# Performance work log

Hardware: AMD Instinct MI355X
Metric: run time of the kernel (lower is better)

## Reference

```python
import jax, jax.numpy as jnp
import numpy as np
import math

NUM_HEADS = 16
HEAD_DIM = 64  # 1024 / 16

def setup_inputs() -> dict:
    key = jax.random.key(0)
    k1, k2, k3 = jax.random.split(key, 3)
    B, S, D = 2, 2048, 1024
    scale = 1.0 / math.sqrt(D)
    return {
        "hidden_states": jax.random.normal(k1, (B, S, D), dtype=jnp.float32),
        "attention_mask": jnp.ones((B, S), dtype=jnp.int32),
        "Wq": jax.random.normal(k2, (D, D), dtype=jnp.float32) * scale,
        "bq": jnp.zeros((D,), dtype=jnp.float32),
        "Wk": jax.random.normal(k3, (D, D), dtype=jnp.float32) * scale,
        "bk": jnp.zeros((D,), dtype=jnp.float32),
    }

def _split_heads(x):
    # [B, S, D] -> [B, H, S, dh]
    B, S, D = x.shape
    return x.reshape(B, S, NUM_HEADS, HEAD_DIM).transpose(0, 2, 1, 3)

def reference(hidden_states, attention_mask, Wq, bq, Wk, bk):
    q = _split_heads(hidden_states @ Wq + bq)           # [B,H,S,dh]
    k = _split_heads(hidden_states @ Wk + bk)           # [B,H,S,dh]
    k = jax.nn.log_sigmoid(q) + q + k                   # fused logsigmoid on q
    k = jax.nn.log_sigmoid(k)                           # second logsigmoid
    # scores = q @ (-k^T) / sqrt(dh)
    scores = -jnp.einsum('bhqd,bhkd->bhqk', q, k) / math.sqrt(HEAD_DIM)
    # mask broadcast [B,1,S,1]: masks QUERY rows (faithful to original)
    mask = (attention_mask[:, None, :, None] == 0)
    scores = jnp.where(mask, -10000.0, scores)
    probs = jax.nn.softmax(scores, axis=-1)             # [B,H,S,S]
    # note: value == query_layer in this module
    ctx = jnp.einsum('bhqk,bhkd->bhqd', probs, q)       # [B,H,S,dh]
    B, H, S, dh = ctx.shape
    return ctx.transpose(0, 2, 1, 3).reshape(B, S, H * dh)
```

## Files before the change

kernel.cpp:

```cpp
#include <hip/hip_runtime.h>
#include <hip/hip_bf16.h>
#include <math.h>

#define B_  2
#define S_  2048
#define D_  1024
#define H_  16
#define DH_ 64
#define M_  (B_ * S_)

typedef __attribute__((ext_vector_type(8))) short bf16x8;
typedef __attribute__((ext_vector_type(4))) float f32x4;
typedef __attribute__((ext_vector_type(16))) float f32x16;
typedef __attribute__((ext_vector_type(2))) unsigned u32x2;

__device__ __forceinline__ float fast_exp2(float x) {
  return __builtin_amdgcn_exp2f(x);
}

__device__ __forceinline__ unsigned short f2bf(float f) {
  union { float f; unsigned u; } c; c.f = f;
  unsigned u = c.u;
  return (unsigned short)((u + 0x7FFFu + ((u >> 16) & 1u)) >> 16);
}

__device__ __forceinline__ unsigned cvtpk(float lo, float hi) {
  unsigned r;
  asm("v_cvt_pk_bf16_f32 %0, %1, %2" : "=v"(r) : "v"(lo), "v"(hi));
  return r;
}

__device__ __forceinline__ void plswap(unsigned &x, unsigned &y) {
  u32x2 r = __builtin_amdgcn_permlane32_swap(x, y, false, false);
  x = r[0]; y = r[1];
}

__device__ __forceinline__ float logsig(float x) {
  const float e = __expf(-fabsf(x));
  return fminf(x, 0.f) - __logf(1.f + e);
}

__global__ __launch_bounds__(256) void prep_w(
    const float* __restrict__ Wq, const float* __restrict__ Wk,
    unsigned short* __restrict__ WqT, unsigned short* __restrict__ WkT)
{
  __shared__ unsigned short T[64][72];
  const int tid = threadIdx.x;
  const int k0 = blockIdx.x * 64;
  const int n0 = blockIdx.y * 64;
  const float* W = blockIdx.z ? Wk : Wq;
  unsigned short* WT = blockIdx.z ? WkT : WqT;

  const int kr = tid >> 2, nc = (tid & 3) * 16;
  #pragma unroll
  for (int i = 0; i < 4; i++) {
    const float4 v = *(const float4*)&W[(size_t)(k0 + kr) * D_ + n0 + nc + i * 4];
    T[nc + i * 4 + 0][kr] = f2bf(v.x);
    T[nc + i * 4 + 1][kr] = f2bf(v.y);
    T[nc + i * 4 + 2][kr] = f2bf(v.z);
    T[nc + i * 4 + 3][kr] = f2bf(v.w);
  }
  __syncthreads();
  const int nr = tid >> 2, kc = (tid & 3) * 16;
  const uint4 a = *(const uint4*)&T[nr][kc];
  const uint4 b = *(const uint4*)&T[nr][kc + 8];
  *(uint4*)&WT[(size_t)(n0 + nr) * D_ + k0 + kc] = a;
  *(uint4*)&WT[(size_t)(n0 + nr) * D_ + k0 + kc + 8] = b;
}

__global__ __launch_bounds__(512, 4) void proj_kernel(
    const float* __restrict__ hs,
    const unsigned short* __restrict__ WqT, const unsigned short* __restrict__ WkT,
    const float* __restrict__ bqv, const float* __restrict__ bkv,
    unsigned short* __restrict__ K2b, unsigned short* __restrict__ QT)
{
  __shared__ unsigned short Ash[128][72];
  __shared__ unsigned short Bsh[2][64][72];

  const int tid  = threadIdx.x;
  const int w    = tid >> 6;
  const int lane = tid & 63;
  const int quad = lane >> 4;
  const int l16  = lane & 15;
  const int m0 = blockIdx.x * 128;
  const int n0 = blockIdx.y * 64;

  float bqs[4], bks[4];
  #pragma unroll
  for (int nt = 0; nt < 4; nt++) {
    bqs[nt] = bqv[n0 + nt * 16 + l16];
    bks[nt] = bkv[n0 + nt * 16 + l16];
  }

  f32x4 accQ[4], accK[4];
  #pragma unroll
  for (int nt = 0; nt < 4; nt++) {
    accQ[nt] = (f32x4){0.f, 0.f, 0.f, 0.f};
    accK[nt] = (f32x4){0.f, 0.f, 0.f, 0.f};
  }

  const int am = tid >> 2, ac = (tid & 3) * 16;
  const int bn = tid >> 3, bc = (tid & 7) * 8;

  float4 Af[4];
  uint4 Bq, Bk;
  {
    const size_t ra = (size_t)(m0 + am) * D_ + ac;
    #pragma unroll
    for (int i = 0; i < 4; i++) Af[i] = *(const float4*)&hs[ra + i * 4];
    const size_t rb = (size_t)(n0 + bn) * D_ + bc;
    Bq = *(const uint4*)&WqT[rb];
    Bk = *(const uint4*)&WkT[rb];
  }

  for (int k0 = 0; k0 < D_; k0 += 64) {
    if (k0) __syncthreads();
    {
      uint4 t0, t1;
      t0.x = cvtpk(Af[0].x, Af[0].y);  t0.y = cvtpk(Af[0].z, Af[0].w);
      t0.z = cvtpk(Af[1].x, Af[1].y);  t0.w = cvtpk(Af[1].z, Af[1].w);
      t1.x = cvtpk(Af[2].x, Af[2].y);  t1.y = cvtpk(Af[2].z, Af[2].w);
      t1.z = cvtpk(Af[3].x, Af[3].y);  t1.w = cvtpk(Af[3].z, Af[3].w);
      *(uint4*)&Ash[am][ac]     = t0;
      *(uint4*)&Ash[am][ac + 8] = t1;
    }
    *(uint4*)&Bsh[0][bn][bc] = Bq;
    *(uint4*)&Bsh[1][bn][bc] = Bk;
    __syncthreads();

    if (k0 + 64 < D_) {
      const size_t ra = (size_t)(m0 + am) * D_ + (k0 + 64) + ac;
      #pragma unroll
      for (int i = 0; i < 4; i++) Af[i] = *(const float4*)&hs[ra + i * 4];
      const size_t rb = (size_t)(n0 + bn) * D_ + (k0 + 64) + bc;
      Bq = *(const uint4*)&WqT[rb];
      Bk = *(const uint4*)&WkT[rb];
    }

    #pragma unroll
    for (int kk = 0; kk < 2; kk++) {
      const bf16x8 af = *(const bf16x8*)&Ash[w * 16 + l16][kk * 32 + quad * 8];
      #pragma unroll
      for (int nt = 0; nt < 4; nt++) {
        const bf16x8 bq = *(const bf16x8*)&Bsh[0][nt * 16 + l16][kk * 32 + quad * 8];
        const bf16x8 bk = *(const bf16x8*)&Bsh[1][nt * 16 + l16][kk * 32 + quad * 8];
        accQ[nt] = __builtin_amdgcn_mfma_f32_16x16x32_bf16(af, bq, accQ[nt], 0, 0, 0);
        accK[nt] = __builtin_amdgcn_mfma_f32_16x16x32_bf16(af, bk, accK[nt], 0, 0, 0);
      }
    }
  }
  __syncthreads();

  unsigned short* Qt = &Bsh[0][0][0];
  #pragma unroll
  for (int nt = 0; nt < 4; nt++) {
    float qv[4];
    #pragma unroll
    for (int r = 0; r < 4; r++) {
      const float q  = accQ[nt][r] + bqs[nt];
      const float kr = accK[nt][r] + bks[nt];
      const float k2 = logsig(logsig(q) + q + kr);
      const int m = m0 + w * 16 + quad * 4 + r;
      K2b[(size_t)m * D_ + n0 + nt * 16 + l16] = f2bf(k2);
      qv[r] = q;
    }
    const ushort4 qu = {f2bf(qv[0]), f2bf(qv[1]), f2bf(qv[2]), f2bf(qv[3])};
    *(ushort4*)&Qt[(nt * 16 + l16) * 136 + w * 16 + quad * 4] = qu;
  }
  __syncthreads();
  {
    const int dr = tid >> 3, mc = (tid & 7) * 16;
    #pragma unroll
    for (int i = 0; i < 2; i++) {
      const uint4 v = *(const uint4*)&Qt[dr * 136 + mc + i * 8];
      *(uint4*)&QT[(size_t)(n0 + dr) * M_ + m0 + mc + i * 8] = v;
    }
  }
}

__global__ __launch_bounds__(1024) void attn_kernel(
    const unsigned short* __restrict__ QT,
    const unsigned short* __restrict__ K2b,
    const int* __restrict__ mask,
    float* __restrict__ out)
{
  __shared__ unsigned short Qa [256][72];
  __shared__ unsigned short K2s[64][72];
  __shared__ unsigned short Vt [64][72];

  const int tid  = threadIdx.x;
  const int w    = tid >> 6;
  const int lane = tid & 63;
  const int r31  = lane & 31;
  const int hi   = lane >> 5;
  const int hi8  = hi * 8;
  const int qsub = w & 7;
  const int ksel = w >> 3;

  const int qt = blockIdx.x;
  const int bh = blockIdx.y;
  const int b = bh >> 4, h = bh & 15;
  const size_t qrow0 = (size_t)b * S_ + (size_t)qt * 256;
  const size_t krow0 = (size_t)b * S_;
  const size_t trow  = (size_t)h * 64;

  const int rr = tid >> 4, cc = (tid & 15) * 4;
  uint2 kreg, vreg;
  kreg = *(const uint2*)&K2b[(krow0 + rr) * D_ + trow + cc];
  vreg = *(const uint2*)&QT [(trow + rr) * M_ + krow0 + cc];

  {
    const int dr = tid >> 4, qg = tid & 15;
    const int qc = qg * 16;
    const int dcol = dr ^ ((qg & 7) << 3);
    #pragma unroll
    for (int i = 0; i < 2; i++) {
      const uint4 v = *(const uint4*)&QT[(trow + dr) * M_ + qrow0 + qc + i * 8];
      const unsigned short* p = (const unsigned short*)&v;
      #pragma unroll
      for (int j = 0; j < 8; j++) Qa[qc + i * 8 + j][dcol] = p[j];
    }
  }
  __syncthreads();

  bf16x8 qfrag[4];
  {
    const int qrow = qsub * 32 + r31;
    const int g7 = (qrow >> 4) & 7;
    #pragma unroll
    for (int s = 0; s < 4; s++)
      qfrag[s] = *(const bf16x8*)&Qa[qrow][(s * 16 + hi8) ^ (g7 << 3)];
  }

  const float c2 = (mask[qrow0 + qsub * 32 + r31] != 0) ? -0.18033688f : 0.f;
  float rl = 0.f;

  f32x16 Ot0, Ot1;
  #pragma unroll
  for (int r = 0; r < 16; r++) { Ot0[r] = 0.f; Ot1[r] = 0.f; }

  const int NT = S_ / 64;
  for (int kt = 0; kt < NT; kt++) {
    __syncthreads();
    *(uint2*)&K2s[rr][cc] = kreg;
    *(uint2*)&Vt [rr][cc] = vreg;
    __syncthreads();

    if (kt + 1 < NT) {
      kreg = *(const uint2*)&K2b[(krow0 + (kt + 1) * 64 + rr) * D_ + trow + cc];
      vreg = *(const uint2*)&QT [(trow + rr) * M_ + krow0 + (kt + 1) * 64 + cc];
    }

    bf16x8 kf[4];
    #pragma unroll
    for (int s = 0; s < 4; s++)
      kf[s] = *(const bf16x8*)&K2s[ksel * 32 + r31][s * 16 + hi8];
    f32x16 sc;
    #pragma unroll
    for (int r = 0; r < 16; r++) sc[r] = 0.f;
    __builtin_amdgcn_s_setprio(1);
    #pragma unroll
    for (int s = 0; s < 4; s++)
      sc = __builtin_amdgcn_mfma_f32_32x32x16_bf16(kf[s], qfrag[s], sc, 0, 0, 0);
    __builtin_amdgcn_s_setprio(0);

    float p[16];
    #pragma unroll
    for (int r = 0; r < 16; r++) p[r] = fast_exp2(fmaf(sc[r], c2, -12.f));
    #pragma unroll
    for (int r = 0; r < 16; r += 4) rl += ((p[r] + p[r+1]) + (p[r+2] + p[r+3]));

    unsigned pk0 = cvtpk(p[0],  p[1]),  pk1 = cvtpk(p[2],  p[3]);
    unsigned pk2 = cvtpk(p[4],  p[5]),  pk3 = cvtpk(p[6],  p[7]);
    unsigned pk4 = cvtpk(p[8],  p[9]),  pk5 = cvtpk(p[10], p[11]);
    unsigned pk6 = cvtpk(p[12], p[13]), pk7 = cvtpk(p[14], p[15]);
    plswap(pk0, pk2);
    plswap(pk1, pk3);
    plswap(pk4, pk6);
    plswap(pk5, pk7);
    union { unsigned d[8]; bf16x8 v[2]; } pu;
    pu.d[0] = pk0; pu.d[1] = pk1; pu.d[2] = pk2; pu.d[3] = pk3;
    pu.d[4] = pk4; pu.d[5] = pk5; pu.d[6] = pk6; pu.d[7] = pk7;

    __builtin_amdgcn_s_setprio(1);
    #pragma unroll
    for (int s2 = 0; s2 < 2; s2++) {
      const bf16x8 pf  = pu.v[s2];
      const bf16x8 vf0 = *(const bf16x8*)&Vt[r31]     [ksel * 32 + s2 * 16 + hi8];
      const bf16x8 vf1 = *(const bf16x8*)&Vt[32 + r31][ksel * 32 + s2 * 16 + hi8];
      Ot0 = __builtin_amdgcn_mfma_f32_32x32x16_bf16(vf0, pf, Ot0, 0, 0, 0);
      Ot1 = __builtin_amdgcn_mfma_f32_32x32x16_bf16(vf1, pf, Ot1, 0, 0, 0);
    }
    __builtin_amdgcn_s_setprio(0);
  }

  rl += __shfl_xor(rl, 32);
  __syncthreads();
  float* redO = (float*)&Qa[0][0];
  float* redL = (float*)&K2s[0][0];
  if (ksel == 1) {
    #pragma unroll
    for (int r = 0; r < 16; r++) redO[(qsub * 16 + r) * 64 + lane] = Ot0[r];
    redL[qsub * 64 + lane] = rl;
  }
  __syncthreads();
  float inv = 0.f;
  size_t orow = 0;
  if (ksel == 0) {
    const float lt = rl + redL[qsub * 64 + lane];
    inv = 1.f / fmaxf(lt, 1e-35f);
    orow = (qrow0 + qsub * 32 + r31) * D_ + trow;
    #pragma unroll
    for (int rq = 0; rq < 4; rq++) {
      float4 o;
      o.x = (Ot0[4*rq+0] + redO[(qsub*16 + 4*rq+0)*64 + lane]) * inv;
      o.y = (Ot0[4*rq+1] + redO[(qsub*16 + 4*rq+1)*64 + lane]) * inv;
      o.z = (Ot0[4*rq+2] + redO[(qsub*16 + 4*rq+2)*64 + lane]) * inv;
      o.w = (Ot0[4*rq+3] + redO[(qsub*16 + 4*rq+3)*64 + lane]) * inv;
      *(float4*)&out[orow + rq * 8 + 4 * hi] = o;
    }
  }
  __syncthreads();
  if (ksel == 1) {
    #pragma unroll
    for (int r = 0; r < 16; r++) redO[(qsub * 16 + r) * 64 + lane] = Ot1[r];
  }
  __syncthreads();
  if (ksel == 0) {
    #pragma unroll
    for (int rq = 0; rq < 4; rq++) {
      float4 o;
      o.x = (Ot1[4*rq+0] + redO[(qsub*16 + 4*rq+0)*64 + lane]) * inv;
      o.y = (Ot1[4*rq+1] + redO[(qsub*16 + 4*rq+1)*64 + lane]) * inv;
      o.z = (Ot1[4*rq+2] + redO[(qsub*16 + 4*rq+2)*64 + lane]) * inv;
      o.w = (Ot1[4*rq+3] + redO[(qsub*16 + 4*rq+3)*64 + lane]) * inv;
      *(float4*)&out[orow + 32 + rq * 8 + 4 * hi] = o;
    }
  }
}

extern "C" void kernel_launch(void* const* d_in, const int* in_sizes, int n_in,
                              void* d_out, int out_size, void* d_ws, size_t ws_size,
                              hipStream_t stream) {
  const float* hs  = (const float*)d_in[0];
  const int*   msk = (const int*)d_in[1];
  const float* Wq  = (const float*)d_in[2];
  const float* bq  = (const float*)d_in[3];
  const float* Wk  = (const float*)d_in[4];
  const float* bk  = (const float*)d_in[5];
  float* out = (float*)d_out;

  unsigned short* QT  = (unsigned short*)d_ws;
  unsigned short* K2b = QT  + (size_t)D_ * M_;
  unsigned short* WqT = K2b + (size_t)M_ * D_;
  unsigned short* WkT = WqT + (size_t)D_ * D_;

  prep_w<<<dim3(D_ / 64, D_ / 64, 2), 256, 0, stream>>>(Wq, Wk, WqT, WkT);
  proj_kernel<<<dim3(M_ / 128, D_ / 64), 512, 0, stream>>>(hs, WqT, WkT, bq, bk, K2b, QT);
  attn_kernel<<<dim3(S_ / 256, B_ * H_), 1024, 0, stream>>>(QT, K2b, msk, out);
}
```

Measured before the change: 154.5 us.

## Double-buffer shared-memory tiles in projection and attention kernels to halve barriers

Both the projection GEMM and the attention loop now keep two LDS buffers for the streamed operand tiles. Each iteration writes the next tile into the alternate buffer while computing on the current one, and register prefetch reaches two tiles ahead. This drops each loop from two __syncthreads per iteration to one and lets global loads overlap more compute. In exchange it uses more LDS per block, which may reduce occupancy, notably for proj_kernel with launch_bounds(512,4), and it keeps more registers live.

```diff
diff --git a/kernel.cpp b/kernel.cpp
--- a/kernel.cpp
+++ b/kernel.cpp
@@ -74,8 +74,8 @@
     const float* __restrict__ bqv, const float* __restrict__ bkv,
     unsigned short* __restrict__ K2b, unsigned short* __restrict__ QT)
 {
-  __shared__ unsigned short Ash[128][72];
-  __shared__ unsigned short Bsh[2][64][72];
+  __shared__ unsigned short Ash[2][128][72];
+  __shared__ unsigned short Bsh[2][2][64][72];
 
   const int tid  = threadIdx.x;
   const int w    = tid >> 6;
@@ -104,54 +104,67 @@
 
   float4 Af[4];
   uint4 Bq, Bk;
+  const size_t raBase = (size_t)(m0 + am) * D_ + ac;
+  const size_t rbBase = (size_t)(n0 + bn) * D_ + bc;
+
+  #pragma unroll
+  for (int i = 0; i < 4; i++) Af[i] = *(const float4*)&hs[raBase + i * 4];
+  Bq = *(const uint4*)&WqT[rbBase];
+  Bk = *(const uint4*)&WkT[rbBase];
   {
-    const size_t ra = (size_t)(m0 + am) * D_ + ac;
-    #pragma unroll
-    for (int i = 0; i < 4; i++) Af[i] = *(const float4*)&hs[ra + i * 4];
-    const size_t rb = (size_t)(n0 + bn) * D_ + bc;
-    Bq = *(const uint4*)&WqT[rb];
-    Bk = *(const uint4*)&WkT[rb];
-  }
-
-  for (int k0 = 0; k0 < D_; k0 += 64) {
-    if (k0) __syncthreads();
-    {
+    uint4 t0, t1;
+    t0.x = cvtpk(Af[0].x, Af[0].y);  t0.y = cvtpk(Af[0].z, Af[0].w);
+    t0.z = cvtpk(Af[1].x, Af[1].y);  t0.w = cvtpk(Af[1].z, Af[1].w);
+    t1.x = cvtpk(Af[2].x, Af[2].y);  t1.y = cvtpk(Af[2].z, Af[2].w);
+    t1.z = cvtpk(Af[3].x, Af[3].y);  t1.w = cvtpk(Af[3].z, Af[3].w);
+    *(uint4*)&Ash[0][am][ac]     = t0;
+    *(uint4*)&Ash[0][am][ac + 8] = t1;
+  }
+  *(uint4*)&Bsh[0][0][bn][bc] = Bq;
+  *(uint4*)&Bsh[0][1][bn][bc] = Bk;
+  #pragma unroll
+  for (int i = 0; i < 4; i++) Af[i] = *(const float4*)&hs[raBase + 64 + i * 4];
+  Bq = *(const uint4*)&WqT[rbBase + 64];
+  Bk = *(const uint4*)&WkT[rbBase + 64];
+  __syncthreads();
+
+  for (int t = 0; t < D_ / 64; t++) {
+    const int cur = t & 1;
+    if (t + 1 < D_ / 64) {
       uint4 t0, t1;
       t0.x = cvtpk(Af[0].x, Af[0].y);  t0.y = cvtpk(Af[0].z, Af[0].w);
       t0.z = cvtpk(Af[1].x, Af[1].y);  t0.w = cvtpk(Af[1].z, Af[1].w);
       t1.x = cvtpk(Af[2].x, Af[2].y);  t1.y = cvtpk(Af[2].z, Af[2].w);
       t1.z = cvtpk(Af[3].x, Af[3].y);  t1.w = cvtpk(Af[3].z, Af[3].w);
-      *(uint4*)&Ash[am][ac]     = t0;
-      *(uint4*)&Ash[am][ac + 8] = t1;
-    }
-    *(uint4*)&Bsh[0][bn][bc] = Bq;
-    *(uint4*)&Bsh[1][bn][bc] = Bk;
-    __syncthreads();
-
-    if (k0 + 64 < D_) {
-      const size_t ra = (size_t)(m0 + am) * D_ + (k0 + 64) + ac;
+      *(uint4*)&Ash[cur ^ 1][am][ac]     = t0;
+      *(uint4*)&Ash[cur ^ 1][am][ac + 8] = t1;
+      *(uint4*)&Bsh[cur ^ 1][0][bn][bc] = Bq;
+      *(uint4*)&Bsh[cur ^ 1][1][bn][bc] = Bk;
+    }
+    if (t + 2 < D_ / 64) {
+      const size_t ra = raBase + (size_t)(t + 2) * 64;
       #pragma unroll
       for (int i = 0; i < 4; i++) Af[i] = *(const float4*)&hs[ra + i * 4];
-      const size_t rb = (size_t)(n0 + bn) * D_ + (k0 + 64) + bc;
+      const size_t rb = rbBase + (size_t)(t + 2) * 64;
       Bq = *(const uint4*)&WqT[rb];
       Bk = *(const uint4*)&WkT[rb];
     }
 
     #pragma unroll
     for (int kk = 0; kk < 2; kk++) {
-      const bf16x8 af = *(const bf16x8*)&Ash[w * 16 + l16][kk * 32 + quad * 8];
+      const bf16x8 af = *(const bf16x8*)&Ash[cur][w * 16 + l16][kk * 32 + quad * 8];
       #pragma unroll
       for (int nt = 0; nt < 4; nt++) {
-        const bf16x8 bq = *(const bf16x8*)&Bsh[0][nt * 16 + l16][kk * 32 + quad * 8];
-        const bf16x8 bk = *(const bf16x8*)&Bsh[1][nt * 16 + l16][kk * 32 + quad * 8];
+        const bf16x8 bq = *(const bf16x8*)&Bsh[cur][0][nt * 16 + l16][kk * 32 + quad * 8];
+        const bf16x8 bk = *(const bf16x8*)&Bsh[cur][1][nt * 16 + l16][kk * 32 + quad * 8];
         accQ[nt] = __builtin_amdgcn_mfma_f32_16x16x32_bf16(af, bq, accQ[nt], 0, 0, 0);
         accK[nt] = __builtin_amdgcn_mfma_f32_16x16x32_bf16(af, bk, accK[nt], 0, 0, 0);
       }
     }
-  }
-  __syncthreads();
-
-  unsigned short* Qt = &Bsh[0][0][0];
+    __syncthreads();
+  }
+
+  unsigned short* Qt = &Bsh[0][0][0][0];
   #pragma unroll
   for (int nt = 0; nt < 4; nt++) {
     float qv[4];
@@ -185,8 +198,8 @@
     float* __restrict__ out)
 {
   __shared__ unsigned short Qa [256][72];
-  __shared__ unsigned short K2s[64][72];
-  __shared__ unsigned short Vt [64][72];
+  __shared__ unsigned short K2s[2][64][72];
+  __shared__ unsigned short Vt [2][64][72];
 
   const int tid  = threadIdx.x;
   const int w    = tid >> 6;
@@ -221,6 +234,10 @@
       for (int j = 0; j < 8; j++) Qa[qc + i * 8 + j][dcol] = p[j];
     }
   }
+  *(uint2*)&K2s[0][rr][cc] = kreg;
+  *(uint2*)&Vt [0][rr][cc] = vreg;
+  kreg = *(const uint2*)&K2b[(krow0 + 64 + rr) * D_ + trow + cc];
+  vreg = *(const uint2*)&QT [(trow + rr) * M_ + krow0 + 64 + cc];
   __syncthreads();
 
   bf16x8 qfrag[4];
@@ -241,20 +258,22 @@
 
   const int NT = S_ / 64;
   for (int kt = 0; kt < NT; kt++) {
-    __syncthreads();
-    *(uint2*)&K2s[rr][cc] = kreg;
-    *(uint2*)&Vt [rr][cc] = vreg;
-    __syncthreads();
+    const int cur = kt & 1;
+
+    bf16x8 kf[4];
+    #pragma unroll
+    for (int s = 0; s < 4; s++)
+      kf[s] = *(const bf16x8*)&K2s[cur][ksel * 32 + r31][s * 16 + hi8];
 
     if (kt + 1 < NT) {
-      kreg = *(const uint2*)&K2b[(krow0 + (kt + 1) * 64 + rr) * D_ + trow + cc];
-      vreg = *(const uint2*)&QT [(trow + rr) * M_ + krow0 + (kt + 1) * 64 + cc];
-    }
-
-    bf16x8 kf[4];
-    #pragma unroll
-    for (int s = 0; s < 4; s++)
-      kf[s] = *(const bf16x8*)&K2s[ksel * 32 + r31][s * 16 + hi8];
+      *(uint2*)&K2s[cur ^ 1][rr][cc] = kreg;
+      *(uint2*)&Vt [cur ^ 1][rr][cc] = vreg;
+    }
+    if (kt + 2 < NT) {
+      kreg = *(const uint2*)&K2b[(krow0 + (kt + 2) * 64 + rr) * D_ + trow + cc];
+      vreg = *(const uint2*)&QT [(trow + rr) * M_ + krow0 + (kt + 2) * 64 + cc];
+    }
+
     f32x16 sc;
     #pragma unroll
     for (int r = 0; r < 16; r++) sc[r] = 0.f;
@@ -286,18 +305,19 @@
     #pragma unroll
     for (int s2 = 0; s2 < 2; s2++) {
       const bf16x8 pf  = pu.v[s2];
-      const bf16x8 vf0 = *(const bf16x8*)&Vt[r31]     [ksel * 32 + s2 * 16 + hi8];
-      const bf16x8 vf1 = *(const bf16x8*)&Vt[32 + r31][ksel * 32 + s2 * 16 + hi8];
+      const bf16x8 vf0 = *(const bf16x8*)&Vt[cur][r31]     [ksel * 32 + s2 * 16 + hi8];
+      const bf16x8 vf1 = *(const bf16x8*)&Vt[cur][32 + r31][ksel * 32 + s2 * 16 + hi8];
       Ot0 = __builtin_amdgcn_mfma_f32_32x32x16_bf16(vf0, pf, Ot0, 0, 0, 0);
       Ot1 = __builtin_amdgcn_mfma_f32_32x32x16_bf16(vf1, pf, Ot1, 0, 0, 0);
     }
     __builtin_amdgcn_s_setprio(0);
+
+    __syncthreads();
   }
 
   rl += __shfl_xor(rl, 32);
-  __syncthreads();
   float* redO = (float*)&Qa[0][0];
-  float* redL = (float*)&K2s[0][0];
+  float* redL = (float*)&K2s[0][0][0];
   if (ksel == 1) {
     #pragma unroll
     for (int r = 0; r < 16; r++) redO[(qsub * 16 + r) * 64 + lane] = Ot0[r];
```

After: 157.0 us. About the same (+1.6%).
